# Kernel tuning notes

Hardware: AMD Instinct MI355X
Metric: run time of the kernel (lower is better)

## Reference

```python
import jax, jax.numpy as jnp
import numpy as np

B, C, H, W = 64, 512, 64, 64
E, K = 16, 4


def setup_inputs() -> dict:
    key = jax.random.key(0)
    kx, k0, kb0, k1, kb1 = jax.random.split(key, 5)
    scale = 1.0 / np.sqrt(C)
    return {
        "x": jax.random.normal(kx, (B, C, H, W), dtype=jnp.float32),
        "W0": jax.random.normal(k0, (E, C), dtype=jnp.float32) * scale,
        "b0": jax.random.normal(kb0, (E,), dtype=jnp.float32) * scale,
        # NOTE: original zeros fc1.weight at init; we use small random weights so the
        # noise-normalization path is numerically non-degenerate (std>0).
        "W1": jax.random.normal(k1, (E, C), dtype=jnp.float32) * scale,
        "b1": jax.random.normal(kb1, (E,), dtype=jnp.float32) * scale,
    }


def reference(x, W0, b0, W1, b1):
    # Adaptive max + avg pool to 1x1 -> [B, C]
    pooled = jnp.max(x, axis=(2, 3)) + jnp.mean(x, axis=(2, 3))
    # fc0 + LeakyReLU(0.2)
    h = pooled @ W0.T + b0                      # [B, E]
    h = jnp.where(h >= 0, h, 0.2 * h)
    # fc1 -> softplus noise, normalize per-row (torch.std uses ddof=1)
    noise = jax.nn.softplus(pooled @ W1.T + b1)  # [B, E]
    mu = jnp.mean(noise, axis=1, keepdims=True)
    sd = jnp.std(noise, axis=1, keepdims=True, ddof=1)
    norm_noise = (noise - mu) / sd
    # top-k selection on h + norm_noise, mask non-selected with -inf, softmax
    _, topk_idx = jax.lax.top_k(h + norm_noise, K)        # [B, K] int
    mask = jnp.zeros((B, E), dtype=bool).at[jnp.arange(B)[:, None], topk_idx].set(True)
    logits = jnp.where(mask, h, -jnp.inf)
    gate = jax.nn.softmax(logits, axis=1)
    return gate
```

## Files before the change

kernel.cpp:

```cpp
#include <hip/hip_runtime.h>
#include <math.h>


#define HW 4096
#define CC 512
#define EE 16
#define KK 4

__global__ __launch_bounds__(256) void pool_kernel(const float* __restrict__ x,
                                                   float* __restrict__ pooled) {
    const int bc = blockIdx.x;
    const float4* xp = (const float4*)(x + (size_t)bc * HW);
    float mx = -INFINITY, sm = 0.f;
#pragma unroll
    for (int i = 0; i < 4; ++i) {
        float4 v = xp[threadIdx.x + i * 256];
        mx = fmaxf(mx, fmaxf(fmaxf(v.x, v.y), fmaxf(v.z, v.w)));
        sm += (v.x + v.y) + (v.z + v.w);
    }
#pragma unroll
    for (int off = 32; off > 0; off >>= 1) {
        mx = fmaxf(mx, __shfl_down(mx, off, 64));
        sm += __shfl_down(sm, off, 64);
    }
    __shared__ float smx[4], ssm[4];
    const int wave = threadIdx.x >> 6;
    if ((threadIdx.x & 63) == 0) { smx[wave] = mx; ssm[wave] = sm; }
    __syncthreads();
    if (threadIdx.x == 0) {
        mx = fmaxf(fmaxf(smx[0], smx[1]), fmaxf(smx[2], smx[3]));
        sm = (ssm[0] + ssm[1]) + (ssm[2] + ssm[3]);
        pooled[bc] = mx + sm * (1.0f / (float)HW);
    }
}

__global__ __launch_bounds__(256) void gate_kernel(const float* __restrict__ pooled,
                                                   const float* __restrict__ W0,
                                                   const float* __restrict__ b0,
                                                   const float* __restrict__ W1,
                                                   const float* __restrict__ b1,
                                                   float* __restrict__ out) {
    const int b = blockIdx.x;
    __shared__ float sp[CC];
    __shared__ float sh[EE];
    __shared__ float sn[EE];
    sp[threadIdx.x]       = pooled[b * CC + threadIdx.x];
    sp[threadIdx.x + 256] = pooled[b * CC + 256 + threadIdx.x];
    __syncthreads();

    if (threadIdx.x < 2 * EE) {
        const int m = threadIdx.x >> 4;
        const int e = threadIdx.x & 15;
        const float* Wrow = (m ? W1 : W0) + e * CC;
        float acc = 0.f;
#pragma unroll 8
        for (int c = 0; c < CC; ++c) acc = fmaf(sp[c], Wrow[c], acc);
        if (m == 0) {
            acc += b0[e];
            sh[e] = (acc >= 0.f) ? acc : 0.2f * acc;
        } else {
            acc += b1[e];
            sn[e] = fmaxf(acc, 0.f) + log1pf(expf(-fabsf(acc)));
        }
    }
    __syncthreads();

    if (threadIdx.x == 0) {
        float mu = 0.f;
#pragma unroll
        for (int e = 0; e < EE; ++e) mu += sn[e];
        mu *= (1.0f / (float)EE);
        float var = 0.f;
#pragma unroll
        for (int e = 0; e < EE; ++e) { float d = sn[e] - mu; var += d * d; }
        const float sd = sqrtf(var * (1.0f / (float)(EE - 1)));
        const float inv_sd = 1.0f / sd;

        float score[EE];
#pragma unroll
        for (int e = 0; e < EE; ++e) score[e] = sh[e] + (sn[e] - mu) * inv_sd;

        bool sel[EE];
#pragma unroll
        for (int e = 0; e < EE; ++e) sel[e] = false;
        for (int k = 0; k < KK; ++k) {
            int best = 0; float bv = -INFINITY;
            for (int e = 0; e < EE; ++e)
                if (!sel[e] && score[e] > bv) { bv = score[e]; best = e; }
            sel[best] = true;
        }

        float hmax = -INFINITY;
        for (int e = 0; e < EE; ++e) if (sel[e]) hmax = fmaxf(hmax, sh[e]);
        float ex[EE]; float den = 0.f;
        for (int e = 0; e < EE; ++e) {
            ex[e] = sel[e] ? expf(sh[e] - hmax) : 0.f;
            den += ex[e];
        }
        const float inv_den = 1.0f / den;
        for (int e = 0; e < EE; ++e) out[b * EE + e] = ex[e] * inv_den;
    }
}

extern "C" void kernel_launch(void* const* d_in, const int* in_sizes, int n_in,
                              void* d_out, int out_size, void* d_ws, size_t ws_size,
                              hipStream_t stream) {
    const float* x  = (const float*)d_in[0];
    const float* W0 = (const float*)d_in[1];
    const float* b0 = (const float*)d_in[2];
    const float* W1 = (const float*)d_in[3];
    const float* b1 = (const float*)d_in[4];
    float* out = (float*)d_out;
    float* pooled = (float*)d_ws;

    const int B = 64;
    pool_kernel<<<B * CC, 256, 0, stream>>>(x, pooled);
    gate_kernel<<<B, 256, 0, stream>>>(pooled, W0, b0, W1, b1, out);
}
```

Baseline: 683.7 us.

## Pool rows per wave with multiple rows per block; parallelize gate GEMV

The pooling kernel now assigns one row per wave, with each block covering 16 rows. This replaces one block per row followed by a shared-memory reduction, removing the block barrier and cutting the launch to 2048 blocks. The gate kernel spreads each expert dot product across 8 lanes using float4 loads and a shuffle reduction, instead of 32 threads doing serial 512-length loops. The cost is fewer, longer-lived blocks, which may reduce the number of memory requests in flight per CU.

```diff
diff --git a/kernel.cpp b/kernel.cpp
--- a/kernel.cpp
+++ b/kernel.cpp
@@ -6,31 +6,30 @@
 #define CC 512
 #define EE 16
 #define KK 4
+#define ROWS_PER_BLOCK 16
 
 __global__ __launch_bounds__(256) void pool_kernel(const float* __restrict__ x,
                                                    float* __restrict__ pooled) {
-    const int bc = blockIdx.x;
-    const float4* xp = (const float4*)(x + (size_t)bc * HW);
-    float mx = -INFINITY, sm = 0.f;
+    const int wave = threadIdx.x >> 6;
+    const int lane = threadIdx.x & 63;
+    const int base_row = blockIdx.x * ROWS_PER_BLOCK;
 #pragma unroll
-    for (int i = 0; i < 4; ++i) {
-        float4 v = xp[threadIdx.x + i * 256];
-        mx = fmaxf(mx, fmaxf(fmaxf(v.x, v.y), fmaxf(v.z, v.w)));
-        sm += (v.x + v.y) + (v.z + v.w);
-    }
+    for (int i = 0; i < ROWS_PER_BLOCK / 4; ++i) {
+        const int row = base_row + i * 4 + wave;
+        const float4* xp = (const float4*)(x + (size_t)row * HW);
+        float mx = -INFINITY, sm = 0.f;
 #pragma unroll
-    for (int off = 32; off > 0; off >>= 1) {
-        mx = fmaxf(mx, __shfl_down(mx, off, 64));
-        sm += __shfl_down(sm, off, 64);
-    }
-    __shared__ float smx[4], ssm[4];
-    const int wave = threadIdx.x >> 6;
-    if ((threadIdx.x & 63) == 0) { smx[wave] = mx; ssm[wave] = sm; }
-    __syncthreads();
-    if (threadIdx.x == 0) {
-        mx = fmaxf(fmaxf(smx[0], smx[1]), fmaxf(smx[2], smx[3]));
-        sm = (ssm[0] + ssm[1]) + (ssm[2] + ssm[3]);
-        pooled[bc] = mx + sm * (1.0f / (float)HW);
+        for (int j = 0; j < 16; ++j) {
+            float4 v = xp[lane + j * 64];
+            mx = fmaxf(mx, fmaxf(fmaxf(v.x, v.y), fmaxf(v.z, v.w)));
+            sm += (v.x + v.y) + (v.z + v.w);
+        }
+#pragma unroll
+        for (int off = 32; off > 0; off >>= 1) {
+            mx = fmaxf(mx, __shfl_down(mx, off, 64));
+            sm += __shfl_down(sm, off, 64);
+        }
+        if (lane == 0) pooled[row] = mx + sm * (1.0f / (float)HW);
     }
 }
 
@@ -41,26 +40,39 @@
                                                    const float* __restrict__ b1,
                                                    float* __restrict__ out) {
     const int b = blockIdx.x;
-    __shared__ float sp[CC];
+    __shared__ float4 sp[CC / 4];
     __shared__ float sh[EE];
     __shared__ float sn[EE];
-    sp[threadIdx.x]       = pooled[b * CC + threadIdx.x];
-    sp[threadIdx.x + 256] = pooled[b * CC + 256 + threadIdx.x];
+
+    if (threadIdx.x < CC / 4)
+        sp[threadIdx.x] = ((const float4*)(pooled + b * CC))[threadIdx.x];
     __syncthreads();
 
-    if (threadIdx.x < 2 * EE) {
-        const int m = threadIdx.x >> 4;
-        const int e = threadIdx.x & 15;
-        const float* Wrow = (m ? W1 : W0) + e * CC;
-        float acc = 0.f;
-#pragma unroll 8
-        for (int c = 0; c < CC; ++c) acc = fmaf(sp[c], Wrow[c], acc);
+    const int g = threadIdx.x >> 3;
+    const int t = threadIdx.x & 7;
+    const int m = g >> 4;
+    const int e = g & 15;
+    const float4* W4 = (const float4*)((m ? W1 : W0) + e * CC);
+    float acc = 0.f;
+#pragma unroll
+    for (int j = 0; j < 16; ++j) {
+        const float4 w = W4[t + j * 8];
+        const float4 p = sp[t + j * 8];
+        acc = fmaf(w.x, p.x, acc);
+        acc = fmaf(w.y, p.y, acc);
+        acc = fmaf(w.z, p.z, acc);
+        acc = fmaf(w.w, p.w, acc);
+    }
+    acc += __shfl_xor(acc, 4, 64);
+    acc += __shfl_xor(acc, 2, 64);
+    acc += __shfl_xor(acc, 1, 64);
+    if (t == 0) {
         if (m == 0) {
-            acc += b0[e];
-            sh[e] = (acc >= 0.f) ? acc : 0.2f * acc;
+            const float v = acc + b0[e];
+            sh[e] = (v >= 0.f) ? v : 0.2f * v;
         } else {
-            acc += b1[e];
-            sn[e] = fmaxf(acc, 0.f) + log1pf(expf(-fabsf(acc)));
+            const float v = acc + b1[e];
+            sn[e] = fmaxf(v, 0.f) + log1pf(expf(-fabsf(v)));
         }
     }
     __syncthreads();
@@ -68,37 +80,37 @@
     if (threadIdx.x == 0) {
         float mu = 0.f;
 #pragma unroll
-        for (int e = 0; e < EE; ++e) mu += sn[e];
+        for (int e2 = 0; e2 < EE; ++e2) mu += sn[e2];
         mu *= (1.0f / (float)EE);
         float var = 0.f;
 #pragma unroll
-        for (int e = 0; e < EE; ++e) { float d = sn[e] - mu; var += d * d; }
+        for (int e2 = 0; e2 < EE; ++e2) { float d = sn[e2] - mu; var += d * d; }
         const float sd = sqrtf(var * (1.0f / (float)(EE - 1)));
         const float inv_sd = 1.0f / sd;
 
         float score[EE];
 #pragma unroll
-        for (int e = 0; e < EE; ++e) score[e] = sh[e] + (sn[e] - mu) * inv_sd;
+        for (int e2 = 0; e2 < EE; ++e2) score[e2] = sh[e2] + (sn[e2] - mu) * inv_sd;
 
         bool sel[EE];
 #pragma unroll
-        for (int e = 0; e < EE; ++e) sel[e] = false;
+        for (int e2 = 0; e2 < EE; ++e2) sel[e2] = false;
         for (int k = 0; k < KK; ++k) {
             int best = 0; float bv = -INFINITY;
-            for (int e = 0; e < EE; ++e)
-                if (!sel[e] && score[e] > bv) { bv = score[e]; best = e; }
+            for (int e2 = 0; e2 < EE; ++e2)
+                if (!sel[e2] && score[e2] > bv) { bv = score[e2]; best = e2; }
             sel[best] = true;
         }
 
         float hmax = -INFINITY;
-        for (int e = 0; e < EE; ++e) if (sel[e]) hmax = fmaxf(hmax, sh[e]);
+        for (int e2 = 0; e2 < EE; ++e2) if (sel[e2]) hmax = fmaxf(hmax, sh[e2]);
         float ex[EE]; float den = 0.f;
-        for (int e = 0; e < EE; ++e) {
-            ex[e] = sel[e] ? expf(sh[e] - hmax) : 0.f;
-            den += ex[e];
+        for (int e2 = 0; e2 < EE; ++e2) {
+            ex[e2] = sel[e2] ? expf(sh[e2] - hmax) : 0.f;
+            den += ex[e2];
         }
         const float inv_den = 1.0f / den;
-        for (int e = 0; e < EE; ++e) out[b * EE + e] = ex[e] * inv_den;
+        for (int e2 = 0; e2 < EE; ++e2) out[b * EE + e2] = ex[e2] * inv_den;
     }
 }
 
@@ -114,6 +126,6 @@
     float* pooled = (float*)d_ws;
 
     const int B = 64;
-    pool_kernel<<<B * CC, 256, 0, stream>>>(x, pooled);
+    pool_kernel<<<(B * CC) / ROWS_PER_BLOCK, 256, 0, stream>>>(x, pooled);
     gate_kernel<<<B, 256, 0, stream>>>(pooled, W0, b0, W1, b1, out);
 }
```

Result: no change. 676.6 us (-1.0%).
